# Optimization experiments

Hardware: AMD Instinct MI355X
Metric: run time of the kernel (lower is better)

The kernel has to match this reference:

```python
import jax, jax.numpy as jnp
import numpy as np


def setup_inputs() -> dict:
    key = jax.random.key(0)
    k1, _ = jax.random.split(key)
    B, H, W, C = 8, 128, 128, 512
    inputs = jax.random.normal(k1, (B, H, W, C), dtype=jnp.float32)
    gamma = jnp.ones((), dtype=jnp.float32)
    return {"inputs": inputs, "gamma": gamma}


def reference(inputs, gamma):
    B, H, W, C = inputs.shape
    q = inputs.reshape(B, H * W, C).astype(jnp.float32)  # [B, HW, C]
    # attention = key @ query = q^T q  -> [B, C, C]
    attn = jnp.einsum('bnc,bnd->bcd', q, q)
    # reversed-softmax trick: softmax(max - attn) over last axis
    attn = jnp.max(attn, axis=-1, keepdims=True) - attn
    attn = jax.nn.softmax(attn, axis=-1)
    # value = query @ attention -> [B, HW, C]
    value = jnp.einsum('bnc,bcd->bnd', q, attn)
    value = value.astype(inputs.dtype).reshape(B, H, W, C)
    return gamma * value + inputs
```

## Files before the change

kernel.cpp:

```cpp
#include <hip/hip_runtime.h>
#include <hip/hip_bf16.h>

#define B_  8
#define C_  512
#define NN  16384
#define SPL 8
#define KB_ (NN / SPL)
#define TT  (KB_ / 64)

typedef _Float16 half8 __attribute__((ext_vector_type(8)));
typedef float    f32x4 __attribute__((ext_vector_type(4)));

__device__ __forceinline__ unsigned short f2h(float x) {
    union { _Float16 h; unsigned short u; } cv;
    cv.h = (_Float16)x;
    return cv.u;
}

__device__ __forceinline__ void gload16(const unsigned short* src, unsigned short* ldst) {
    __builtin_amdgcn_global_load_lds(
        (const __attribute__((address_space(1))) void*)src,
        (__attribute__((address_space(3))) void*)ldst,
        16, 0, 0);
}

__global__ void ws_probe_kernel(float* out, float v) { out[0] = v; }

__global__ __launch_bounds__(256) void pack_kernel(const float* __restrict__ in,
                                                   unsigned short* __restrict__ qT,
                                                   unsigned short* __restrict__ qn) {
    __shared__ unsigned short lh[64][72];
    int t  = threadIdx.x;
    int n0 = blockIdx.x * 64;
    int c0 = blockIdx.y * 64;
    int b  = blockIdx.z;
    const float* ib = in + ((size_t)b * NN + n0) * C_ + c0;

    int nl0 = (t >> 3) * 2;
    int cl  = (t & 7) * 8;
    const float* s0 = ib + (size_t)nl0 * C_ + cl;
    const float* s1 = s0 + C_;
    float4 a0 = *(const float4*)s0,  a1 = *(const float4*)(s0 + 4);
    float4 b0 = *(const float4*)s1,  b1 = *(const float4*)(s1 + 4);
    unsigned short q0[8] __attribute__((aligned(16)));
    unsigned short q1[8] __attribute__((aligned(16)));
    q0[0] = f2h(a0.x); q0[1] = f2h(a0.y); q0[2] = f2h(a0.z); q0[3] = f2h(a0.w);
    q0[4] = f2h(a1.x); q0[5] = f2h(a1.y); q0[6] = f2h(a1.z); q0[7] = f2h(a1.w);
    q1[0] = f2h(b0.x); q1[1] = f2h(b0.y); q1[2] = f2h(b0.z); q1[3] = f2h(b0.w);
    q1[4] = f2h(b1.x); q1[5] = f2h(b1.y); q1[6] = f2h(b1.z); q1[7] = f2h(b1.w);
    *(uint4*)(qn + ((size_t)b * NN + n0 + nl0) * C_ + c0 + cl)     = *(const uint4*)q0;
    *(uint4*)(qn + ((size_t)b * NN + n0 + nl0 + 1) * C_ + c0 + cl) = *(const uint4*)q1;
#pragma unroll
    for (int j = 0; j < 8; ++j) {
        int r = cl + j;
        int col = nl0 ^ (((r >> 3) & 3) << 3);
        ushort2 w; w.x = q0[j]; w.y = q1[j];
        *(ushort2*)&lh[r][col] = w;
    }
    __syncthreads();
    size_t obase = ((size_t)b * C_ + c0) * NN + n0;
#pragma unroll
    for (int p = 0; p < 2; ++p) {
        int cr = p * 32 + (t >> 3);
        int nf = (t & 7) * 8;
        int nfx = nf ^ (((cr >> 3) & 3) << 3);
        *(uint4*)(qT + obase + (size_t)cr * NN + nf) = *(const uint4*)&lh[cr][nfx];
    }
}

__global__ __launch_bounds__(512, 2) void gram_kernel(const unsigned short* __restrict__ qT,
                                                      float* __restrict__ P) {
    __shared__ unsigned short sA[2][16384];
    __shared__ unsigned short sB[2][16384];
    int t = threadIdx.x, lane = t & 63, wave = t >> 6;
    int wr = wave >> 2, wc = wave & 3;
    int bid = blockIdx.x;
    int b = bid & 7, r = bid >> 3;
    int tile = r & 3, split = r >> 2;
    int tc = tile >> 1, td = tile & 1;
    size_t qb = (size_t)b * C_ * NN;
    const unsigned short* Ap = qT + qb + (size_t)(tc * 256) * NN + (size_t)split * KB_;
    const unsigned short* Bp = qT + qb + (size_t)(td * 256) * NN + (size_t)split * KB_;

    f32x4 acc[8][4];
#pragma unroll
    for (int m = 0; m < 8; ++m)
#pragma unroll
        for (int n = 0; n < 4; ++n) acc[m][n] = (f32x4){0.f, 0.f, 0.f, 0.f};

    int o0 = t * 16,         u0 = o0 ^ (((o0 >> 7) & 7) << 4);
    int o1 = (t + 512) * 16, u1 = o1 ^ (((o1 >> 7) & 7) << 4);
    int rih0 = u0 >> 7, k0 = (u0 & 127) >> 1;
    int rih1 = u1 >> 7, k1 = (u1 & 127) >> 1;

#define STAGE(dst, dd, h, panel, kt)                                                        \
    do {                                                                                    \
        gload16((panel) + (size_t)((h)*128 + rih0) * NN + (kt)*64 + k0,                     \
                &dst[dd][(h)*8192 + t * 8]);                                                \
        gload16((panel) + (size_t)((h)*128 + rih1) * NN + (kt)*64 + k1,                     \
                &dst[dd][(h)*8192 + (t + 512) * 8]);                                        \
    } while (0)

    int g16 = (lane >> 4) * 16;
#define AFRAG(dd, row, ks) \
    (*(const half8*)((const char*)&sA[dd][0] + (((row)*128 + (ks)*64 + g16) ^ (((row)&7) << 4))))
#define BFRAG(dd, row, ks) \
    (*(const half8*)((const char*)&sB[dd][0] + (((row)*128 + (ks)*64 + g16) ^ (((row)&7) << 4))))

    STAGE(sA, 0, 0, Ap, 0);
    STAGE(sB, 0, 0, Bp, 0);
    STAGE(sB, 0, 1, Bp, 0);
    STAGE(sA, 0, 1, Ap, 0);
    asm volatile("s_waitcnt vmcnt(2)" ::: "memory");
    __builtin_amdgcn_s_barrier();

    for (int kt = 0; kt < TT; ++kt) {
        int d = kt & 1, nd = d ^ 1;
        half8 aF[4][2], b0F[2][2], b1F[2][2];
#pragma unroll
        for (int m = 0; m < 4; ++m) {
            int row = wr * 64 + m * 16 + (lane & 15);
#pragma unroll
            for (int ks = 0; ks < 2; ++ks) aF[m][ks] = AFRAG(d, row, ks);
        }
#pragma unroll
        for (int n = 0; n < 2; ++n) {
            int row0 = wc * 32 + n * 16 + (lane & 15);
#pragma unroll
            for (int ks = 0; ks < 2; ++ks) {
                b0F[n][ks] = BFRAG(d, row0, ks);
                b1F[n][ks] = BFRAG(d, (row0 + 128), ks);
            }
        }
        if (kt + 1 < TT) {
            STAGE(sA, nd, 0, Ap, kt + 1);
            STAGE(sB, nd, 0, Bp, kt + 1);
            STAGE(sB, nd, 1, Bp, kt + 1);
        }
        __builtin_amdgcn_s_setprio(1);
#pragma unroll
        for (int m = 0; m < 4; ++m)
#pragma unroll
            for (int n = 0; n < 2; ++n)
#pragma unroll
                for (int ks = 0; ks < 2; ++ks) {
                    acc[m][n]     = __builtin_amdgcn_mfma_f32_16x16x32_f16(aF[m][ks], b0F[n][ks], acc[m][n],     0, 0, 0);
                    acc[m][n + 2] = __builtin_amdgcn_mfma_f32_16x16x32_f16(aF[m][ks], b1F[n][ks], acc[m][n + 2], 0, 0, 0);
                }
        __builtin_amdgcn_s_setprio(0);
        if (kt + 1 < TT) {
            asm volatile("s_waitcnt vmcnt(6)" ::: "memory");
        } else {
            asm volatile("s_waitcnt vmcnt(0)" ::: "memory");
        }
        __builtin_amdgcn_s_barrier();
#pragma unroll
        for (int m = 0; m < 4; ++m) {
            int row = 128 + wr * 64 + m * 16 + (lane & 15);
#pragma unroll
            for (int ks = 0; ks < 2; ++ks) aF[m][ks] = AFRAG(d, row, ks);
        }
        if (kt + 1 < TT) STAGE(sA, nd, 1, Ap, kt + 1);
        __builtin_amdgcn_s_setprio(1);
#pragma unroll
        for (int m = 0; m < 4; ++m)
#pragma unroll
            for (int n = 0; n < 2; ++n)
#pragma unroll
                for (int ks = 0; ks < 2; ++ks) {
                    acc[m + 4][n + 2] = __builtin_amdgcn_mfma_f32_16x16x32_f16(aF[m][ks], b1F[n][ks], acc[m + 4][n + 2], 0, 0, 0);
                    acc[m + 4][n]     = __builtin_amdgcn_mfma_f32_16x16x32_f16(aF[m][ks], b0F[n][ks], acc[m + 4][n],     0, 0, 0);
                }
        __builtin_amdgcn_s_setprio(0);
        asm volatile("s_waitcnt vmcnt(2)" ::: "memory");
        __builtin_amdgcn_s_barrier();
    }

    float* outp = P + ((size_t)(split * 8 + b)) * (C_ * C_);
#pragma unroll
    for (int m = 0; m < 8; ++m) {
        int row0 = tc * 256 + wr * 64 + (m & 3) * 16 + (m >> 2) * 128 + (lane >> 4) * 4;
#pragma unroll
        for (int n = 0; n < 4; ++n) {
            int col = td * 256 + wc * 32 + (n & 1) * 16 + (n >> 1) * 128 + (lane & 15);
#pragma unroll
            for (int j = 0; j < 4; ++j)
                outp[(size_t)(row0 + j) * C_ + col] = acc[m][n][j];
        }
    }
#undef STAGE
#undef AFRAG
#undef BFRAG
}

__global__ __launch_bounds__(256) void softmax_kernel(const float* __restrict__ P,
                                                      unsigned short* __restrict__ WT) {
    __shared__ unsigned short lw[C_ * 4];
    int t = threadIdx.x, lane = t & 63, wave = t >> 6;
    int b = blockIdx.y;
    int c = blockIdx.x * 4 + wave;
    const float* base = P + (size_t)b * (C_ * C_) + (size_t)c * C_;

    float g[8];
    float mn = 3.4e38f;
#pragma unroll
    for (int k = 0; k < 8; ++k) {
        int d = k * 64 + lane;
        float v = 0.f;
#pragma unroll
        for (int s = 0; s < 8; ++s) v += base[(size_t)s * (8 * C_ * C_) + d];
        g[k] = v;
        mn = fminf(mn, v);
    }
#pragma unroll
    for (int o = 32; o; o >>= 1) mn = fminf(mn, __shfl_xor(mn, o));
    float w[8];
    float sum = 0.f;
#pragma unroll
    for (int k = 0; k < 8; ++k) { w[k] = __expf(mn - g[k]); sum += w[k]; }
#pragma unroll
    for (int o = 32; o; o >>= 1) sum += __shfl_xor(sum, o);
    float inv = 1.0f / sum;
#pragma unroll
    for (int k = 0; k < 8; ++k) {
        int d = k * 64 + lane;
        lw[d * 4 + wave] = f2h(w[k] * inv);
    }
    __syncthreads();
    int c0 = blockIdx.x * 4;
    for (int d = t; d < C_; d += 256)
        *(ushort4*)(WT + ((size_t)b * C_ + d) * C_ + c0) = *(ushort4*)&lw[d * 4];
}

__global__ __launch_bounds__(512, 4) void value_kernel(const unsigned short* __restrict__ qn,
                                                       const unsigned short* __restrict__ WT,
                                                       const float* __restrict__ gamma,
                                                       float* __restrict__ out) {
    __shared__ unsigned short smem[36864];
    unsigned short* sAb = smem;
    unsigned short* sBb = smem + 12288;
    int t = threadIdx.x, lane = t & 63, wave = t >> 6;
    int wr = wave >> 2, wc = wave & 3;
    int bid = blockIdx.x;
    int b = bid & 7, r = bid >> 3;
    int dt = r & 1, nt = r >> 1;
    const unsigned short* Ap = qn + ((size_t)b * NN + (size_t)nt * 128) * C_;
    const unsigned short* Bp = WT + ((size_t)b * C_ + dt * 256) * C_;

    f32x4 acc[4][4];
#pragma unroll
    for (int m = 0; m < 4; ++m)
#pragma unroll
        for (int n = 0; n < 4; ++n) acc[m][n] = (f32x4){0.f, 0.f, 0.f, 0.f};

    int arow = t >> 2;
    int aswz = ((t & 3) ^ ((t >> 3) & 3)) * 8;

    auto stage = [&](int buf, int s) {
        gload16(Ap + (size_t)arow * C_ + s * 32 + aswz, &sAb[buf * 4096 + t * 8]);
        gload16(Bp + (size_t)arow * C_ + s * 32 + aswz, &sBb[buf * 8192 + t * 8]);
        gload16(Bp + (size_t)(arow + 128) * C_ + s * 32 + aswz, &sBb[buf * 8192 + 4096 + t * 8]);
    };

    stage(0, 0);
    stage(1, 1);
    asm volatile("s_waitcnt vmcnt(3)" ::: "memory");
    __builtin_amdgcn_s_barrier();

    int slot = lane >> 4;
    int l15 = lane & 15;
    int i0 = 0, i1 = 1, i2 = 2;

#pragma unroll 1
    for (int s = 0; s < 16; ++s) {
        const unsigned short* pa = sAb + (size_t)i0 * 4096;
        const unsigned short* pb = sBb + (size_t)i0 * 8192;
        half8 aF[4];
#pragma unroll
        for (int m = 0; m < 4; ++m) {
            int row = wr * 64 + m * 16 + l15;
            aF[m] = *(const half8*)(pa + row * 32 + ((slot ^ ((row >> 1) & 3)) * 8));
        }
        if (s + 2 < 16) stage(i2, s + 2);
        __builtin_amdgcn_s_setprio(1);
#pragma unroll
        for (int n = 0; n < 4; ++n) {
            int row = wc * 64 + n * 16 + l15;
            half8 bF = *(const half8*)(pb + row * 32 + ((slot ^ ((row >> 1) & 3)) * 8));
#pragma unroll
            for (int m = 0; m < 4; ++m)
                acc[m][n] = __builtin_amdgcn_mfma_f32_16x16x32_f16(aF[m], bF, acc[m][n], 0, 0, 0);
        }
        __builtin_amdgcn_s_setprio(0);
        if (s < 15) {
            if (s + 2 < 16) {
                asm volatile("s_waitcnt vmcnt(3)" ::: "memory");
            } else {
                asm volatile("s_waitcnt vmcnt(0)" ::: "memory");
            }
            __builtin_amdgcn_s_barrier();
        }
        int tmp = i0; i0 = i1; i1 = i2; i2 = tmp;
    }

    float gm = gamma[0];
    float* ebuf = (float*)smem;
    const int ES = 132;
    size_t rowg0 = (size_t)b * NN + (size_t)nt * 128;
    int colg0 = dt * 256;

#pragma unroll
    for (int p = 0; p < 2; ++p) {
        __builtin_amdgcn_s_barrier();
        if ((wc >> 1) == p) {
            int cb = (wc & 1) * 64;
#pragma unroll
            for (int m = 0; m < 4; ++m) {
                int row0 = wr * 64 + m * 16 + (lane >> 4) * 4;
#pragma unroll
                for (int n = 0; n < 4; ++n) {
                    int col = cb + n * 16 + l15;
#pragma unroll
                    for (int j = 0; j < 4; ++j)
                        ebuf[(row0 + j) * ES + col] = acc[m][n][j];
                }
            }
        }
        __builtin_amdgcn_s_barrier();
#pragma unroll
        for (int it = 0; it < 4; ++it) {
            int row = (t >> 4) + it * 32;
            int col = (t & 15) * 8;
            f32x4 v0 = *(const f32x4*)&ebuf[row * ES + col];
            f32x4 v1 = *(const f32x4*)&ebuf[row * ES + col + 4];
            size_t g = (rowg0 + row) * C_ + colg0 + p * 128 + col;
            uint4 qv = *(const uint4*)&qn[g];
            const _Float16* qh = (const _Float16*)&qv;
            float4 o0, o1;
            o0.x = gm * v0[0] + (float)qh[0]; o0.y = gm * v0[1] + (float)qh[1];
            o0.z = gm * v0[2] + (float)qh[2]; o0.w = gm * v0[3] + (float)qh[3];
            o1.x = gm * v1[0] + (float)qh[4]; o1.y = gm * v1[1] + (float)qh[5];
            o1.z = gm * v1[2] + (float)qh[6]; o1.w = gm * v1[3] + (float)qh[7];
            *(float4*)&out[g] = o0;
            *(float4*)&out[g + 4] = o1;
        }
    }
}

extern "C" void kernel_launch(void* const* d_in, const int* in_sizes, int n_in,
                              void* d_out, int out_size, void* d_ws, size_t ws_size,
                              hipStream_t stream) {
    const float* in    = (const float*)d_in[0];
    const float* gamma = (const float*)d_in[1];
    float* out = (float*)d_out;

    const size_t q_elems = (size_t)B_ * C_ * NN;
    const size_t p_elems = (size_t)B_ * C_ * C_;
    const size_t need = q_elems * 2
                      + q_elems * 2
                      + (size_t)SPL * p_elems * 4
                      + p_elems * 2;
    if (ws_size < need) {
        ws_probe_kernel<<<1, 1, 0, stream>>>(out, (float)ws_size);
        return;
    }

    unsigned short* qT = (unsigned short*)d_ws;
    unsigned short* qn = qT + q_elems;
    float* P = (float*)(qn + q_elems);
    unsigned short* WT = (unsigned short*)(P + (size_t)SPL * p_elems);

    pack_kernel<<<dim3(NN / 64, C_ / 64, B_), 256, 0, stream>>>(in, qT, qn);
    gram_kernel<<<256, 512, 0, stream>>>(qT, P);
    softmax_kernel<<<dim3(C_ / 4, B_), 256, 0, stream>>>(P, WT);
    value_kernel<<<2048, 512, 0, stream>>>(qn, WT, gamma, out);
}
```

Measured before the change: 328.0 us.

## Shrink gram tile to 128x256, triple-buffer K=32 stages, double grid

The Gram kernel's output tile shrinks from 256x256 to 128x256 per block. The K step drops from 64 to 32 with a three-deep LDS ring buffer, and the grid doubles to 512 blocks. LDS use and accumulator registers fall, so launch bounds now ask for 4 blocks per CU, aiming at more occupancy and better latency hiding. In exchange, arithmetic intensity per loaded byte drops because the A tile is smaller, and each MFMA gets more barriers.

```diff
diff --git a/kernel.cpp b/kernel.cpp
--- a/kernel.cpp
+++ b/kernel.cpp
@@ -6,7 +6,6 @@
 #define NN  16384
 #define SPL 8
 #define KB_ (NN / SPL)
-#define TT  (KB_ / 64)
 
 typedef _Float16 half8 __attribute__((ext_vector_type(8)));
 typedef float    f32x4 __attribute__((ext_vector_type(4)));
@@ -68,129 +67,90 @@
     }
 }
 
-__global__ __launch_bounds__(512, 2) void gram_kernel(const unsigned short* __restrict__ qT,
+__global__ __launch_bounds__(512, 4) void gram_kernel(const unsigned short* __restrict__ qT,
                                                       float* __restrict__ P) {
-    __shared__ unsigned short sA[2][16384];
-    __shared__ unsigned short sB[2][16384];
+    __shared__ unsigned short smem[36864];
+    unsigned short* sAb = smem;
+    unsigned short* sBb = smem + 12288;
     int t = threadIdx.x, lane = t & 63, wave = t >> 6;
     int wr = wave >> 2, wc = wave & 3;
     int bid = blockIdx.x;
     int b = bid & 7, r = bid >> 3;
-    int tile = r & 3, split = r >> 2;
-    int tc = tile >> 1, td = tile & 1;
+    int tile = r & 7, split = r >> 3;
+    int tr = tile >> 1, tcol = tile & 1;
     size_t qb = (size_t)b * C_ * NN;
-    const unsigned short* Ap = qT + qb + (size_t)(tc * 256) * NN + (size_t)split * KB_;
-    const unsigned short* Bp = qT + qb + (size_t)(td * 256) * NN + (size_t)split * KB_;
-
-    f32x4 acc[8][4];
-#pragma unroll
-    for (int m = 0; m < 8; ++m)
+    const unsigned short* Ap = qT + qb + (size_t)(tr * 128) * NN + (size_t)split * KB_;
+    const unsigned short* Bp = qT + qb + (size_t)(tcol * 256) * NN + (size_t)split * KB_;
+
+    f32x4 acc[4][4];
+#pragma unroll
+    for (int m = 0; m < 4; ++m)
 #pragma unroll
         for (int n = 0; n < 4; ++n) acc[m][n] = (f32x4){0.f, 0.f, 0.f, 0.f};
 
-    int o0 = t * 16,         u0 = o0 ^ (((o0 >> 7) & 7) << 4);
-    int o1 = (t + 512) * 16, u1 = o1 ^ (((o1 >> 7) & 7) << 4);
-    int rih0 = u0 >> 7, k0 = (u0 & 127) >> 1;
-    int rih1 = u1 >> 7, k1 = (u1 & 127) >> 1;
-
-#define STAGE(dst, dd, h, panel, kt)                                                        \
-    do {                                                                                    \
-        gload16((panel) + (size_t)((h)*128 + rih0) * NN + (kt)*64 + k0,                     \
-                &dst[dd][(h)*8192 + t * 8]);                                                \
-        gload16((panel) + (size_t)((h)*128 + rih1) * NN + (kt)*64 + k1,                     \
-                &dst[dd][(h)*8192 + (t + 512) * 8]);                                        \
-    } while (0)
-
-    int g16 = (lane >> 4) * 16;
-#define AFRAG(dd, row, ks) \
-    (*(const half8*)((const char*)&sA[dd][0] + (((row)*128 + (ks)*64 + g16) ^ (((row)&7) << 4))))
-#define BFRAG(dd, row, ks) \
-    (*(const half8*)((const char*)&sB[dd][0] + (((row)*128 + (ks)*64 + g16) ^ (((row)&7) << 4))))
-
-    STAGE(sA, 0, 0, Ap, 0);
-    STAGE(sB, 0, 0, Bp, 0);
-    STAGE(sB, 0, 1, Bp, 0);
-    STAGE(sA, 0, 1, Ap, 0);
-    asm volatile("s_waitcnt vmcnt(2)" ::: "memory");
+    int arow = t >> 2;
+    int aswz = ((t & 3) ^ ((t >> 3) & 3)) * 8;
+
+    auto stage = [&](int buf, int s) {
+        gload16(Ap + (size_t)arow * NN + s * 32 + aswz, &sAb[buf * 4096 + t * 8]);
+        gload16(Bp + (size_t)arow * NN + s * 32 + aswz, &sBb[buf * 8192 + t * 8]);
+        gload16(Bp + (size_t)(arow + 128) * NN + s * 32 + aswz, &sBb[buf * 8192 + 4096 + t * 8]);
+    };
+
+    stage(0, 0);
+    stage(1, 1);
+    asm volatile("s_waitcnt vmcnt(3)" ::: "memory");
     __builtin_amdgcn_s_barrier();
 
-    for (int kt = 0; kt < TT; ++kt) {
-        int d = kt & 1, nd = d ^ 1;
-        half8 aF[4][2], b0F[2][2], b1F[2][2];
+    int slot = lane >> 4;
+    int l15 = lane & 15;
+    int i0 = 0, i1 = 1, i2 = 2;
+    const int NS = KB_ / 32;
+
+#pragma unroll 1
+    for (int s = 0; s < NS; ++s) {
+        const unsigned short* pa = sAb + (size_t)i0 * 4096;
+        const unsigned short* pb = sBb + (size_t)i0 * 8192;
+        half8 aF[4];
 #pragma unroll
         for (int m = 0; m < 4; ++m) {
-            int row = wr * 64 + m * 16 + (lane & 15);
-#pragma unroll
-            for (int ks = 0; ks < 2; ++ks) aF[m][ks] = AFRAG(d, row, ks);
-        }
-#pragma unroll
-        for (int n = 0; n < 2; ++n) {
-            int row0 = wc * 32 + n * 16 + (lane & 15);
-#pragma unroll
-            for (int ks = 0; ks < 2; ++ks) {
-                b0F[n][ks] = BFRAG(d, row0, ks);
-                b1F[n][ks] = BFRAG(d, (row0 + 128), ks);
+            int row = wr * 64 + m * 16 + l15;
+            aF[m] = *(const half8*)(pa + row * 32 + ((slot ^ ((row >> 1) & 3)) * 8));
+        }
+        if (s + 2 < NS) stage(i2, s + 2);
+        __builtin_amdgcn_s_setprio(1);
+#pragma unroll
+        for (int n = 0; n < 4; ++n) {
+            int row = wc * 64 + n * 16 + l15;
+            half8 bF = *(const half8*)(pb + row * 32 + ((slot ^ ((row >> 1) & 3)) * 8));
+#pragma unroll
+            for (int m = 0; m < 4; ++m)
+                acc[m][n] = __builtin_amdgcn_mfma_f32_16x16x32_f16(aF[m], bF, acc[m][n], 0, 0, 0);
+        }
+        __builtin_amdgcn_s_setprio(0);
+        if (s < NS - 1) {
+            if (s + 2 < NS) {
+                asm volatile("s_waitcnt vmcnt(3)" ::: "memory");
+            } else {
+                asm volatile("s_waitcnt vmcnt(0)" ::: "memory");
             }
-        }
-        if (kt + 1 < TT) {
-            STAGE(sA, nd, 0, Ap, kt + 1);
-            STAGE(sB, nd, 0, Bp, kt + 1);
-            STAGE(sB, nd, 1, Bp, kt + 1);
-        }
-        __builtin_amdgcn_s_setprio(1);
-#pragma unroll
-        for (int m = 0; m < 4; ++m)
-#pragma unroll
-            for (int n = 0; n < 2; ++n)
-#pragma unroll
-                for (int ks = 0; ks < 2; ++ks) {
-                    acc[m][n]     = __builtin_amdgcn_mfma_f32_16x16x32_f16(aF[m][ks], b0F[n][ks], acc[m][n],     0, 0, 0);
-                    acc[m][n + 2] = __builtin_amdgcn_mfma_f32_16x16x32_f16(aF[m][ks], b1F[n][ks], acc[m][n + 2], 0, 0, 0);
-                }
-        __builtin_amdgcn_s_setprio(0);
-        if (kt + 1 < TT) {
-            asm volatile("s_waitcnt vmcnt(6)" ::: "memory");
-        } else {
-            asm volatile("s_waitcnt vmcnt(0)" ::: "memory");
-        }
-        __builtin_amdgcn_s_barrier();
-#pragma unroll
-        for (int m = 0; m < 4; ++m) {
-            int row = 128 + wr * 64 + m * 16 + (lane & 15);
-#pragma unroll
-            for (int ks = 0; ks < 2; ++ks) aF[m][ks] = AFRAG(d, row, ks);
-        }
-        if (kt + 1 < TT) STAGE(sA, nd, 1, Ap, kt + 1);
-        __builtin_amdgcn_s_setprio(1);
-#pragma unroll
-        for (int m = 0; m < 4; ++m)
-#pragma unroll
-            for (int n = 0; n < 2; ++n)
-#pragma unroll
-                for (int ks = 0; ks < 2; ++ks) {
-                    acc[m + 4][n + 2] = __builtin_amdgcn_mfma_f32_16x16x32_f16(aF[m][ks], b1F[n][ks], acc[m + 4][n + 2], 0, 0, 0);
-                    acc[m + 4][n]     = __builtin_amdgcn_mfma_f32_16x16x32_f16(aF[m][ks], b0F[n][ks], acc[m + 4][n],     0, 0, 0);
-                }
-        __builtin_amdgcn_s_setprio(0);
-        asm volatile("s_waitcnt vmcnt(2)" ::: "memory");
-        __builtin_amdgcn_s_barrier();
+            __builtin_amdgcn_s_barrier();
+        }
+        int tmp = i0; i0 = i1; i1 = i2; i2 = tmp;
     }
 
     float* outp = P + ((size_t)(split * 8 + b)) * (C_ * C_);
 #pragma unroll
-    for (int m = 0; m < 8; ++m) {
-        int row0 = tc * 256 + wr * 64 + (m & 3) * 16 + (m >> 2) * 128 + (lane >> 4) * 4;
+    for (int m = 0; m < 4; ++m) {
+        int row0 = tr * 128 + wr * 64 + m * 16 + (lane >> 4) * 4;
 #pragma unroll
         for (int n = 0; n < 4; ++n) {
-            int col = td * 256 + wc * 32 + (n & 1) * 16 + (n >> 1) * 128 + (lane & 15);
+            int col = tcol * 256 + wc * 64 + n * 16 + l15;
 #pragma unroll
             for (int j = 0; j < 4; ++j)
                 outp[(size_t)(row0 + j) * C_ + col] = acc[m][n][j];
         }
     }
-#undef STAGE
-#undef AFRAG
-#undef BFRAG
 }
 
 __global__ __launch_bounds__(256) void softmax_kernel(const float* __restrict__ P,
@@ -371,7 +331,7 @@
     unsigned short* WT = (unsigned short*)(P + (size_t)SPL * p_elems);
 
     pack_kernel<<<dim3(NN / 64, C_ / 64, B_), 256, 0, stream>>>(in, qT, qn);
-    gram_kernel<<<256, 512, 0, stream>>>(qT, P);
+    gram_kernel<<<512, 512, 0, stream>>>(qT, P);
     softmax_kernel<<<dim3(C_ / 4, B_), 256, 0, stream>>>(P, WT);
     value_kernel<<<2048, 512, 0, stream>>>(qn, WT, gamma, out);
 }
```

Result: slower. 338.4 us (+3.1%).
